# Performance work log

Measured on AMD Instinct MI355X. Metric: run time of the kernel, lower is better.

The kernel has to match this reference:

```python
import jax, jax.numpy as jnp
import numpy as np
from jax import lax

B, C, A = 32, 84, 8400      # batch, 4+nc channels, anchors (640x640, strides 8/16/32)
NC = 80                     # num classes
K = 1000                    # max_det
CONF_THRES = 0.1
IOU_THRES = 0.7
MAX_WH = 7680.0             # class offset for non-agnostic NMS (ultralytics constant)
SCALE = min(640.0 / 1080.0, 640.0 / 1920.0)  # letterbox scale (input 640, orig 1920x1080)


def setup_inputs() -> dict:
    key = jax.random.key(0)
    k1, k2, k3 = jax.random.split(key, 3)
    # YOLOv8 head output: rows 0:4 are decoded xywh boxes in input pixels, rows 4: are sigmoided class scores
    cxcy = jax.random.uniform(k1, (B, 2, A), jnp.float32, 0.0, 640.0)
    wh = jax.random.uniform(k2, (B, 2, A), jnp.float32, 8.0, 120.0)
    scores = jax.random.uniform(k3, (B, NC, A), jnp.float32, 0.0, 1.0)
    preds = jnp.concatenate([cxcy, wh, scores], axis=1)  # [B, 84, A]
    return {"preds": preds}


def _xywh2xyxy(b):
    cx, cy, w, h = b[:, 0], b[:, 1], b[:, 2], b[:, 3]
    return jnp.stack([cx - w / 2, cy - h / 2, cx + w / 2, cy + h / 2], axis=1)


def _pairwise_iou(b):  # b: [K,4] xyxy
    area = (b[:, 2] - b[:, 0]) * (b[:, 3] - b[:, 1])
    lt = jnp.maximum(b[:, None, :2], b[None, :, :2])
    rb = jnp.minimum(b[:, None, 2:], b[None, :, 2:])
    wh = jnp.clip(rb - lt, 0.0)
    inter = wh[..., 0] * wh[..., 1]
    return inter / (area[:, None] + area[None, :] - inter + 1e-7)


def _nms_per_image(p):  # p: [84, A]
    boxes = _xywh2xyxy(p[:4].T)          # [A,4]
    cls_scores = p[4:]                   # [NC, A]
    conf = jnp.max(cls_scores, axis=0)   # best-class confidence (multi_label=False)
    cls = jnp.argmax(cls_scores, axis=0).astype(jnp.float32)
    # conf threshold + class filter (classes=[0])
    valid = (conf > CONF_THRES) & (cls == 0.0)
    masked = jnp.where(valid, conf, -1.0)
    top_s, idx = lax.top_k(masked, K)    # candidates sorted by score desc
    top_boxes = boxes[idx]               # [K,4]
    top_cls = cls[idx]
    top_valid = top_s > CONF_THRES
    # class-offset boxes for non-agnostic NMS (agnostic=False)
    nms_boxes = top_boxes + top_cls[:, None] * MAX_WH
    iou = _pairwise_iou(nms_boxes)       # [K,K]
    ar = jnp.arange(K)

    def body(i, keep):
        suppress = (iou[i] > IOU_THRES) & keep[i] & (ar > i)
        return keep & ~suppress

    keep = lax.fori_loop(0, K, body, top_valid)
    out_boxes = top_boxes / SCALE        # rescale to original image coords
    out = jnp.concatenate(
        [out_boxes, top_s[:, None], top_cls[:, None]], axis=1)  # [K,6]
    return jnp.where(keep[:, None], out, 0.0)


def reference(preds):
    # [B, K, 6]: x1,y1,x2,y2 (original-image coords), score, class
    return jax.vmap(_nms_per_image)(preds)
```

## Files before the change

### kernel.cpp

```cpp
#include <hip/hip_runtime.h>

#define BATCH 32
#define CH    84
#define NA    8400
#define KTOP  1000
#define MAXC  512
#define NW    (MAXC/64)
#define GROUPS 2100
#define SLICES 9

__global__ __launch_bounds__(256) void cand_kernel(const float* __restrict__ preds,
        int* __restrict__ counts, float* __restrict__ cscore, int* __restrict__ cidx) {
    int blk = blockIdx.x;
    int b = blk / SLICES;
    int slice = blk - b * SLICES;
    int g = slice * 256 + threadIdx.x;

    __shared__ int lcount;
    __shared__ int lbase;
    __shared__ float lsc[1024];
    __shared__ int   lix[1024];
    if (threadIdx.x == 0) lcount = 0;
    __syncthreads();

    if (g < GROUPS) {
        const float* base = preds + (size_t)b * (CH * NA);
        const float4 s0 = *(const float4*)(base + 4 * NA + 4 * g);
        float4 m; m.x = m.y = m.z = m.w = -1.0f;
        #pragma unroll 4
        for (int c = 5; c < CH; ++c) {
            float4 v = *(const float4*)(base + c * NA + 4 * g);
            m.x = fmaxf(m.x, v.x);
            m.y = fmaxf(m.y, v.y);
            m.z = fmaxf(m.z, v.z);
            m.w = fmaxf(m.w, v.w);
        }
        float s[4]  = {s0.x, s0.y, s0.z, s0.w};
        float mm[4] = {m.x, m.y, m.z, m.w};
        #pragma unroll
        for (int k = 0; k < 4; ++k) {
            if (s[k] > 0.1f && s[k] >= mm[k]) {
                int p = atomicAdd(&lcount, 1);
                lsc[p] = s[k];
                lix[p] = 4 * g + k;
            }
        }
    }
    __syncthreads();
    if (threadIdx.x == 0) lbase = atomicAdd(&counts[b], lcount);
    __syncthreads();
    int n = lcount, bs = lbase;
    for (int i = threadIdx.x; i < n; i += 256) {
        int p = bs + i;
        if (p < MAXC) {
            cscore[b * MAXC + p] = lsc[i];
            cidx[b * MAXC + p]   = lix[i];
        }
    }
}

__global__ __launch_bounds__(256) void nms_kernel(const float* __restrict__ preds,
        const int* __restrict__ counts, const float* __restrict__ cscore,
        const int* __restrict__ cidx, float* __restrict__ out) {
    int b = blockIdx.x;
    int tid = threadIdx.x;

    __shared__ float rs[MAXC]; __shared__ int ri[MAXC];
    __shared__ float ss[MAXC]; __shared__ int sa[MAXC];
    __shared__ float x1[MAXC], y1[MAXC], x2[MAXC], y2[MAXC], ar[MAXC];
    __shared__ unsigned long long mask[MAXC][NW];
    __shared__ unsigned long long keepw[NW];

    int n = counts[b];
    if (n > MAXC) n = MAXC;

    for (int i = tid; i < n; i += 256) { rs[i] = cscore[b * MAXC + i]; ri[i] = cidx[b * MAXC + i]; }
    __syncthreads();

    for (int i = tid; i < n; i += 256) {
        float si = rs[i]; int ii = ri[i];
        int r = 0;
        for (int j = 0; j < n; ++j) {
            float sj = rs[j]; int ij = ri[j];
            if (sj > si || (sj == si && ij < ii)) r++;
        }
        ss[r] = si; sa[r] = ii;
    }
    __syncthreads();

    const float* base = preds + (size_t)b * (CH * NA);
    for (int i = tid; i < n; i += 256) {
        int a = sa[i];
        float cx = base[0 * NA + a], cy = base[1 * NA + a];
        float w  = base[2 * NA + a], h  = base[3 * NA + a];
        float hx = w * 0.5f, hy = h * 0.5f;
        float X1 = cx - hx, Y1 = cy - hy, X2 = cx + hx, Y2 = cy + hy;
        x1[i] = X1; y1[i] = Y1; x2[i] = X2; y2[i] = Y2;
        ar[i] = (X2 - X1) * (Y2 - Y1);
    }
    __syncthreads();

    int nw = (n + 63) >> 6;
    for (int t = tid; t < n * nw; t += 256) {
        int i = t / nw;
        int w = t - i * nw;
        int j0 = w * 64;
        int jend = (j0 + 64 < n) ? (j0 + 64) : n;
        int jstart = (j0 > i + 1) ? j0 : (i + 1);
        unsigned long long bits = 0ull;
        float xi1 = x1[i], yi1 = y1[i], xi2 = x2[i], yi2 = y2[i], ai = ar[i];
        for (int j = jstart; j < jend; ++j) {
            float lx = fmaxf(xi1, x1[j]), ly = fmaxf(yi1, y1[j]);
            float rx = fminf(xi2, x2[j]), ry = fminf(yi2, y2[j]);
            float iw = fmaxf(rx - lx, 0.0f), ih = fmaxf(ry - ly, 0.0f);
            float inter = iw * ih;
            float iou = inter / (ai + ar[j] - inter + 1e-7f);
            if (iou > 0.7f) bits |= (1ull << (j - j0));
        }
        mask[i][w] = bits;
    }
    __syncthreads();

    if (tid == 0) {
        unsigned long long kp[NW];
        #pragma unroll
        for (int w = 0; w < NW; ++w) {
            int lo = w * 64;
            if (n >= lo + 64)      kp[w] = ~0ull;
            else if (n <= lo)      kp[w] = 0ull;
            else                   kp[w] = (1ull << (n - lo)) - 1ull;
        }
        for (int i = 0; i < n; ++i) {
            if ((kp[i >> 6] >> (i & 63)) & 1ull) {
                for (int w = (i >> 6); w < nw; ++w) kp[w] &= ~mask[i][w];
            }
        }
        #pragma unroll
        for (int w = 0; w < NW; ++w) keepw[w] = kp[w];
    }
    __syncthreads();

    float* ob = out + (size_t)b * KTOP * 6;
    const float SCALE = (float)(640.0 / 1920.0);
    for (int r = tid; r < KTOP; r += 256) {
        float v0 = 0.f, v1 = 0.f, v2 = 0.f, v3 = 0.f, v4 = 0.f, v5 = 0.f;
        if (r < n && ((keepw[r >> 6] >> (r & 63)) & 1ull)) {
            v0 = x1[r] / SCALE; v1 = y1[r] / SCALE;
            v2 = x2[r] / SCALE; v3 = y2[r] / SCALE;
            v4 = ss[r]; v5 = 0.0f;
        }
        ob[r * 6 + 0] = v0; ob[r * 6 + 1] = v1; ob[r * 6 + 2] = v2;
        ob[r * 6 + 3] = v3; ob[r * 6 + 4] = v4; ob[r * 6 + 5] = v5;
    }
}

extern "C" void kernel_launch(void* const* d_in, const int* in_sizes, int n_in,
                              void* d_out, int out_size, void* d_ws, size_t ws_size,
                              hipStream_t stream) {
    const float* preds = (const float*)d_in[0];
    float* out = (float*)d_out;

    int*   counts = (int*)d_ws;
    float* cscore = (float*)((char*)d_ws + 128);
    int*   cidx   = (int*)((char*)d_ws + 128 + (size_t)BATCH * MAXC * sizeof(float));

    hipMemsetAsync(d_ws, 0, 128, stream);
    cand_kernel<<<BATCH * SLICES, 256, 0, stream>>>(preds, counts, cscore, cidx);
    nms_kernel<<<BATCH, 256, 0, stream>>>(preds, counts, cscore, cidx, out);
}
```

Measured before the change: 174.9 us.

## Split class-max over 4 lanes and replace mask+serial NMS with wave-level scan

The candidate kernel now gives each anchor group to 4 threads, each reducing 20 class channels, and combines them with shuffles. It uses 33 slices instead of 9, so more blocks run in parallel. The NMS kernel drops the precomputed pairwise IoU bitmask and the single-thread serial suppression loop. Instead one 64-lane wave walks the sorted candidates, broadcasts the keep bit by ballot and suppresses boxes held in lane registers, templated on the candidate count. This removes the mask build and the serial one-thread bottleneck, but computes IoU on the fly, which costs a division per box per kept candidate, and leaves three of the block's four waves idle during the scan.

```diff
diff --git a/kernel.cpp b/kernel.cpp
--- a/kernel.cpp
+++ b/kernel.cpp
@@ -5,58 +5,104 @@
 #define NA    8400
 #define KTOP  1000
 #define MAXC  512
-#define NW    (MAXC/64)
 #define GROUPS 2100
-#define SLICES 9
+#define SLICES 33
+#define IOU_T 0.7f
 
 __global__ __launch_bounds__(256) void cand_kernel(const float* __restrict__ preds,
         int* __restrict__ counts, float* __restrict__ cscore, int* __restrict__ cidx) {
-    int blk = blockIdx.x;
-    int b = blk / SLICES;
-    int slice = blk - b * SLICES;
-    int g = slice * 256 + threadIdx.x;
+    int b = blockIdx.x / SLICES;
+    int slice = blockIdx.x - b * SLICES;
+    int t = threadIdx.x;
+    int gl = t >> 2, chunk = t & 3;
+    int g = slice * 64 + gl;
+    bool active = g < GROUPS;
 
-    __shared__ int lcount;
-    __shared__ int lbase;
-    __shared__ float lsc[1024];
-    __shared__ int   lix[1024];
-    if (threadIdx.x == 0) lcount = 0;
+    __shared__ int lcount, lbase;
+    __shared__ float lsc[256];
+    __shared__ int   lix[256];
+    if (t == 0) lcount = 0;
     __syncthreads();
 
-    if (g < GROUPS) {
-        const float* base = preds + (size_t)b * (CH * NA);
-        const float4 s0 = *(const float4*)(base + 4 * NA + 4 * g);
-        float4 m; m.x = m.y = m.z = m.w = -1.0f;
-        #pragma unroll 4
-        for (int c = 5; c < CH; ++c) {
-            float4 v = *(const float4*)(base + c * NA + 4 * g);
-            m.x = fmaxf(m.x, v.x);
-            m.y = fmaxf(m.y, v.y);
-            m.z = fmaxf(m.z, v.z);
-            m.w = fmaxf(m.w, v.w);
+    const float* base = preds + (size_t)b * (CH * NA);
+    float mx = -1.f, my = -1.f, mz = -1.f, mw = -1.f;
+    if (active) {
+        int c0 = 5 + chunk * 20;
+        int c1 = (chunk == 3) ? CH : c0 + 20;
+        const float* p = base + (size_t)c0 * NA + 4 * g;
+        for (int c = c0; c < c1; ++c, p += NA) {
+            float4 v = *(const float4*)p;
+            mx = fmaxf(mx, v.x); my = fmaxf(my, v.y);
+            mz = fmaxf(mz, v.z); mw = fmaxf(mw, v.w);
         }
-        float s[4]  = {s0.x, s0.y, s0.z, s0.w};
-        float mm[4] = {m.x, m.y, m.z, m.w};
+    }
+    mx = fmaxf(mx, __shfl_xor(mx, 1)); my = fmaxf(my, __shfl_xor(my, 1));
+    mz = fmaxf(mz, __shfl_xor(mz, 1)); mw = fmaxf(mw, __shfl_xor(mw, 1));
+    mx = fmaxf(mx, __shfl_xor(mx, 2)); my = fmaxf(my, __shfl_xor(my, 2));
+    mz = fmaxf(mz, __shfl_xor(mz, 2)); mw = fmaxf(mw, __shfl_xor(mw, 2));
+
+    if (active && chunk == 0) {
+        float4 s0 = *(const float4*)(base + (size_t)4 * NA + 4 * g);
+        float s[4] = {s0.x, s0.y, s0.z, s0.w};
+        float m[4] = {mx, my, mz, mw};
         #pragma unroll
         for (int k = 0; k < 4; ++k) {
-            if (s[k] > 0.1f && s[k] >= mm[k]) {
-                int p = atomicAdd(&lcount, 1);
-                lsc[p] = s[k];
-                lix[p] = 4 * g + k;
+            if (s[k] > 0.1f && s[k] >= m[k]) {
+                int p_ = atomicAdd(&lcount, 1);
+                lsc[p_] = s[k];
+                lix[p_] = 4 * g + k;
             }
         }
     }
     __syncthreads();
-    if (threadIdx.x == 0) lbase = atomicAdd(&counts[b], lcount);
+    if (t == 0) lbase = atomicAdd(&counts[b], lcount);
     __syncthreads();
-    int n = lcount, bs = lbase;
-    for (int i = threadIdx.x; i < n; i += 256) {
-        int p = bs + i;
-        if (p < MAXC) {
-            cscore[b * MAXC + p] = lsc[i];
-            cidx[b * MAXC + p]   = lix[i];
+    int nloc = lcount, bs = lbase;
+    for (int i = t; i < nloc; i += 256) {
+        int p_ = bs + i;
+        if (p_ < MAXC) {
+            cscore[b * MAXC + p_] = lsc[i];
+            cidx[b * MAXC + p_]   = lix[i];
         }
     }
+}
+
+template<int S>
+__device__ unsigned int nms_scan(int n, int lane, const float4* bxy, const float* ars) {
+    float ox1[S], oy1[S], ox2[S], oy2[S], oar[S];
+    unsigned int keep = 0u;
+    #pragma unroll
+    for (int k = 0; k < S; ++k) {
+        int c = k * 64 + lane;
+        if (c < n) {
+            float4 v = bxy[c];
+            ox1[k] = v.x; oy1[k] = v.y; ox2[k] = v.z; oy2[k] = v.w;
+            oar[k] = ars[c];
+            keep |= (1u << k);
+        } else {
+            ox1[k] = 0.f; oy1[k] = 0.f; ox2[k] = -1.f; oy2[k] = -1.f; oar[k] = 0.f;
+        }
+    }
+    for (int i = 0; i < n; ++i) {
+        int which = i >> 6, src = i & 63;
+        int mybit = (keep >> which) & 1;
+        unsigned long long bal = __ballot(mybit);
+        if ((bal >> src) & 1ull) {
+            float4 bi = bxy[i];
+            float ai = ars[i];
+            #pragma unroll
+            for (int k = 0; k < S; ++k) {
+                float lx = fmaxf(bi.x, ox1[k]), ly = fmaxf(bi.y, oy1[k]);
+                float rx = fminf(bi.z, ox2[k]), ry = fminf(bi.w, oy2[k]);
+                float iw = fmaxf(rx - lx, 0.0f), ih = fmaxf(ry - ly, 0.0f);
+                float inter = iw * ih;
+                float iou = inter / (ai + oar[k] - inter + 1e-7f);
+                int c = k * 64 + lane;
+                if (c > i && iou > IOU_T) keep &= ~(1u << k);
+            }
+        }
+    }
+    return keep;
 }
 
 __global__ __launch_bounds__(256) void nms_kernel(const float* __restrict__ preds,
@@ -67,9 +113,9 @@
 
     __shared__ float rs[MAXC]; __shared__ int ri[MAXC];
     __shared__ float ss[MAXC]; __shared__ int sa[MAXC];
-    __shared__ float x1[MAXC], y1[MAXC], x2[MAXC], y2[MAXC], ar[MAXC];
-    __shared__ unsigned long long mask[MAXC][NW];
-    __shared__ unsigned long long keepw[NW];
+    __shared__ float4 bxy[MAXC];
+    __shared__ float  ars[MAXC];
+    __shared__ unsigned int keepm[64];
 
     int n = counts[b];
     if (n > MAXC) n = MAXC;
@@ -91,62 +137,32 @@
     const float* base = preds + (size_t)b * (CH * NA);
     for (int i = tid; i < n; i += 256) {
         int a = sa[i];
-        float cx = base[0 * NA + a], cy = base[1 * NA + a];
-        float w  = base[2 * NA + a], h  = base[3 * NA + a];
+        float cx = base[a], cy = base[NA + a];
+        float w  = base[2 * NA + a], h = base[3 * NA + a];
         float hx = w * 0.5f, hy = h * 0.5f;
         float X1 = cx - hx, Y1 = cy - hy, X2 = cx + hx, Y2 = cy + hy;
-        x1[i] = X1; y1[i] = Y1; x2[i] = X2; y2[i] = Y2;
-        ar[i] = (X2 - X1) * (Y2 - Y1);
+        bxy[i] = make_float4(X1, Y1, X2, Y2);
+        ars[i] = (X2 - X1) * (Y2 - Y1);
     }
     __syncthreads();
 
-    int nw = (n + 63) >> 6;
-    for (int t = tid; t < n * nw; t += 256) {
-        int i = t / nw;
-        int w = t - i * nw;
-        int j0 = w * 64;
-        int jend = (j0 + 64 < n) ? (j0 + 64) : n;
-        int jstart = (j0 > i + 1) ? j0 : (i + 1);
-        unsigned long long bits = 0ull;
-        float xi1 = x1[i], yi1 = y1[i], xi2 = x2[i], yi2 = y2[i], ai = ar[i];
-        for (int j = jstart; j < jend; ++j) {
-            float lx = fmaxf(xi1, x1[j]), ly = fmaxf(yi1, y1[j]);
-            float rx = fminf(xi2, x2[j]), ry = fminf(yi2, y2[j]);
-            float iw = fmaxf(rx - lx, 0.0f), ih = fmaxf(ry - ly, 0.0f);
-            float inter = iw * ih;
-            float iou = inter / (ai + ar[j] - inter + 1e-7f);
-            if (iou > 0.7f) bits |= (1ull << (j - j0));
-        }
-        mask[i][w] = bits;
-    }
-    __syncthreads();
-
-    if (tid == 0) {
-        unsigned long long kp[NW];
-        #pragma unroll
-        for (int w = 0; w < NW; ++w) {
-            int lo = w * 64;
-            if (n >= lo + 64)      kp[w] = ~0ull;
-            else if (n <= lo)      kp[w] = 0ull;
-            else                   kp[w] = (1ull << (n - lo)) - 1ull;
-        }
-        for (int i = 0; i < n; ++i) {
-            if ((kp[i >> 6] >> (i & 63)) & 1ull) {
-                for (int w = (i >> 6); w < nw; ++w) kp[w] &= ~mask[i][w];
-            }
-        }
-        #pragma unroll
-        for (int w = 0; w < NW; ++w) keepw[w] = kp[w];
+    if (tid < 64) {
+        unsigned int kp;
+        if (n <= 128)      kp = nms_scan<2>(n, tid, bxy, ars);
+        else if (n <= 256) kp = nms_scan<4>(n, tid, bxy, ars);
+        else               kp = nms_scan<8>(n, tid, bxy, ars);
+        keepm[tid] = kp;
     }
     __syncthreads();
 
     float* ob = out + (size_t)b * KTOP * 6;
-    const float SCALE = (float)(640.0 / 1920.0);
+    const float SCALEF = (float)(640.0 / 1920.0);
     for (int r = tid; r < KTOP; r += 256) {
         float v0 = 0.f, v1 = 0.f, v2 = 0.f, v3 = 0.f, v4 = 0.f, v5 = 0.f;
-        if (r < n && ((keepw[r >> 6] >> (r & 63)) & 1ull)) {
-            v0 = x1[r] / SCALE; v1 = y1[r] / SCALE;
-            v2 = x2[r] / SCALE; v3 = y2[r] / SCALE;
+        if (r < n && ((keepm[r & 63] >> (r >> 6)) & 1u)) {
+            float4 bx = bxy[r];
+            v0 = bx.x / SCALEF; v1 = bx.y / SCALEF;
+            v2 = bx.z / SCALEF; v3 = bx.w / SCALEF;
             v4 = ss[r]; v5 = 0.0f;
         }
         ob[r * 6 + 0] = v0; ob[r * 6 + 1] = v1; ob[r * 6 + 2] = v2;
```

Measured after the change: 172.3 us. About the same (-1.5%).
